# Kernel tuning notes

Measured on AMD Instinct MI355X. Metric: run time of the kernel, lower is better.

The kernel has to match this reference:

```python
import jax, jax.numpy as jnp
import numpy as np

SD = 4            # sqrt of capsule dim (matrix pose)
STRIDE = 2
LN_EPS = 1e-5


def _unfold(x, k, s):
    # x: [B, N, H, W, A] -> patches [B, N, k, k, Ho, Wo, A]  (matches torch unfold+permute)
    B, N, H, W, A = x.shape
    Ho = (H - k) // s + 1
    Wo = (W - k) // s + 1
    ih = np.arange(Ho)[:, None] * s + np.arange(k)   # [Ho, k]
    iw = np.arange(Wo)[:, None] * s + np.arange(k)   # [Wo, k]
    p = x[:, :, ih]               # [B, N, Ho, k, W, A]
    p = p[:, :, :, :, iw]         # [B, N, Ho, k, Wo, k, A]
    return p.transpose(0, 1, 3, 5, 2, 4, 6)


def _layer_norm(v, g, b):
    mu = jnp.mean(v, axis=-1, keepdims=True)
    var = jnp.mean(jnp.square(v - mu), axis=-1, keepdims=True)
    return (v - mu) * jax.lax.rsqrt(var + LN_EPS) * g + b


def setup_inputs() -> dict:
    key = jax.random.key(0)
    k0, k1, k2 = jax.random.split(key, 3)
    B, N, H, W, A = 64, 32, 16, 16, 16     # batch, in caps, spatial, pose dim
    K, M, D = 3, 32, 16                     # kernel, out caps (conv), out pose dim
    Ho = Wo = (H - K) // STRIDE + 1         # 7
    Nfc, Cls = M * Ho * Wo, 10              # 1568 fc input caps, 10 classes
    x = jax.random.normal(k0, (B, N, H, W, A), dtype=jnp.float32)
    c_conv = np.sqrt(M / (SD * N * K * K)).astype(np.float32)
    w_conv = c_conv * jax.random.normal(k1, (K, K, N, SD, SD, M), dtype=jnp.float32)
    c_fc = np.sqrt(Cls / (SD * Nfc)).astype(np.float32)
    w_fc = c_fc * jax.random.normal(k2, (Nfc, SD, SD, Cls), dtype=jnp.float32)
    return {
        "x": x, "w_conv": w_conv, "w_fc": w_fc,
        "ln1_g": jnp.ones((D,), jnp.float32), "ln1_b": jnp.zeros((D,), jnp.float32),
        "ln2_g": jnp.ones((D,), jnp.float32), "ln2_b": jnp.zeros((D,), jnp.float32),
        "num_routing": 3,
    }


def reference(x, w_conv, w_fc, ln1_g, ln1_b, ln2_g, ln2_b, num_routing):
    B = x.shape[0]
    K, _, N, _, _, M = w_conv.shape
    D = SD * SD
    scale = 1.0 / np.sqrt(D)

    # ---------------- CapsuleCONV (matrix pose) ----------------
    patches = _unfold(x, K, STRIDE)                       # [B,N,K,K,Ho,Wo,A]
    Ho, Wo = patches.shape[4], patches.shape[5]
    inp = patches.reshape(B, N, K, K, Ho, Wo, SD, SD)     # bnklhwax

    # pass 0: uniform routing prior (softmax of zeros) == 1/M
    v = jnp.einsum('bnklhwax,klnxdm->bmhwad', inp, w_conv) / M
    v = _layer_norm(v.reshape(B, M, Ho, Wo, D), ln1_g, ln1_b)
    for _ in range(num_routing - 1):
        v4 = v.reshape(B, M, Ho, Wo, SD, SD)
        logits = jnp.einsum('bnklhwax,klnxdm,bmhwad->bnklmhw', inp, w_conv, v4) * scale
        qk = jax.nn.softmax(logits, axis=4)
        qk = qk / (jnp.sum(qk, axis=4, keepdims=True) + 1e-10)
        v = jnp.einsum('bnklmhw,bnklhwax,klnxdm->bmhwad', qk, inp, w_conv)
        v = _layer_norm(v.reshape(B, M, Ho, Wo, D), ln1_g, ln1_b)

    # ---------------- CapsuleFC (matrix pose) ----------------
    # [B,M,Ho,Wo,D] -> permute(0,4,1,2,3) -> flatten -> [B, M*Ho*Wo, D]
    fc_in = v.transpose(0, 4, 1, 2, 3).reshape(B, D, M * Ho * Wo).transpose(0, 2, 1)
    Nfc, Cls = w_fc.shape[0], w_fc.shape[3]
    _in = fc_in.reshape(B, Nfc, SD, SD)                   # bnax

    u = jnp.einsum('bnax,nxdm->bmad', _in, w_fc) / Cls
    u = _layer_norm(u.reshape(B, Cls, D), ln2_g, ln2_b)
    for _ in range(num_routing - 1):
        u4 = u.reshape(B, Cls, SD, SD)
        logits = jnp.einsum('bnax,nxdm,bmad->bnm', _in, w_fc, u4) * scale
        qk = jax.nn.softmax(logits, axis=2)
        qk = qk / (jnp.sum(qk, axis=2, keepdims=True) + 1e-10)
        u = jnp.einsum('bnm,bnax,nxdm->bmad', qk, _in, w_fc)
        u = _layer_norm(u.reshape(B, Cls, D), ln2_g, ln2_b)

    return u  # [B, num_classes, out_d_capsules]
```

## Files before the change

### kernel.cpp

```cpp
#include <hip/hip_runtime.h>
#include <hip/hip_bf16.h>


#define LN_EPS 1e-5f

typedef _Float16 h2 __attribute__((ext_vector_type(2)));

__device__ __forceinline__ unsigned packh2(float a, float b) {
    const unsigned short ua = __builtin_bit_cast(unsigned short, (_Float16)a);
    const unsigned short ub = __builtin_bit_cast(unsigned short, (_Float16)b);
    return (unsigned)ua | ((unsigned)ub << 16);
}

__device__ __forceinline__ float fdot2u(unsigned a, unsigned b, float c) {
#if __has_builtin(__builtin_amdgcn_fdot2)
    return __builtin_amdgcn_fdot2(__builtin_bit_cast(h2, a),
                                  __builtin_bit_cast(h2, b), c, false);
#else
    const h2 ha = __builtin_bit_cast(h2, a), hb = __builtin_bit_cast(h2, b);
    return fmaf((float)ha.x, (float)hb.x, fmaf((float)ha.y, (float)hb.y, c));
#endif
}

__global__ __launch_bounds__(256) void transpose_wconv(
    const float* __restrict__ wconv, unsigned short* __restrict__ wTh)
{
    const int i = blockIdx.x * 256 + threadIdx.x;
    if (i < 147456) {
        const int x = i & 3, d = (i >> 2) & 3, mm = (i >> 4) & 31, r = i >> 9;
        const int n = r / 9, kl = r % 9;
        const float v = wconv[((kl * 32 + n) * 16 + x * 4 + d) * 32 + mm];
        wTh[i] = __builtin_bit_cast(unsigned short, (_Float16)v);
    }
}
__global__ __launch_bounds__(256) void transpose_wfc(
    const float* __restrict__ wfc, float* __restrict__ wT2b)
{
    const int j = blockIdx.x * 256 + threadIdx.x;
    if (j < 401408) {
        const int xd = j & 15, mm = (j >> 4) & 15, n = j >> 8;
        const int x = xd >> 2, dd = xd & 3;
        wT2b[j] = (mm < 10) ? wfc[((n * 4 + x) * 4 + dd) * 10 + mm] : 0.f;
    }
}
__global__ __launch_bounds__(256) void transpose_weights(
    const float* __restrict__ wconv, const float* __restrict__ wfc,
    unsigned short* __restrict__ wTh, float* __restrict__ wT2b)
{
    const int blk = blockIdx.x;
    if (blk < 576) {
        const int i = blk * 256 + threadIdx.x;
        if (i < 147456) {
            const int x = i & 3, d = (i >> 2) & 3, mm = (i >> 4) & 31, r = i >> 9;
            const int n = r / 9, kl = r % 9;
            const float v = wconv[((kl * 32 + n) * 16 + x * 4 + d) * 32 + mm];
            wTh[i] = __builtin_bit_cast(unsigned short, (_Float16)v);
        }
    } else {
        const int j = (blk - 576) * 256 + threadIdx.x;
        if (j < 401408) {
            const int xd = j & 15, mm = (j >> 4) & 15, n = j >> 8;
            const int x = xd >> 2, dd = xd & 3;
            wT2b[j] = (mm < 10) ? wfc[((n * 4 + x) * 4 + dd) * 10 + mm] : 0.f;
        }
    }
}

__global__ __launch_bounds__(256, 4) void conv_routing_kernel(
    const float* __restrict__ x,
    const unsigned short* __restrict__ wTh,
    const float* __restrict__ ln1g,
    const float* __restrict__ ln1b,
    const int*   __restrict__ nroute,
    float* __restrict__ vout)
{
    __shared__ unsigned short s_inp[288][16];
    __shared__ float s_v[32][17];
    __shared__ float s_red[2][32][17];

    const int tid = threadIdx.x;
    const int m   = tid & 31;
    const int g   = (tid >> 5) & 7;
    const int lw  = tid >> 6;
    const int site = blockIdx.x;
    const int b = site / 49, hw = site % 49;
    const int h = hw / 7, w = hw % 7;

    for (int i = tid; i < 1152; i += 256) {
        const int row = i >> 2, q = i & 3;
        const int n = row / 9, kl = row % 9;
        const int k = kl / 3, l = kl % 3;
        const float4 val = *(const float4*)(
            x + ((((b * 32 + n) * 16 + (2 * h + k)) * 16 + (2 * w + l)) * 16 + q * 4));
        uint2 p;
        p.x = packh2(val.x, val.y);
        p.y = packh2(val.z, val.w);
        *(uint2*)(&s_inp[row][q * 4]) = p;
    }
    __syncthreads();

    const int R = *nroute;
    const int nkl0 = g * 36;
    const unsigned short* const wp0 = wTh + (nkl0 * 32 + m) * 16;

    for (int pass = 0; pass < R; ++pass) {
        float vn[16];
#pragma unroll
        for (int i = 0; i < 16; ++i) vn[i] = 0.f;

        if (pass == 0) {
            const unsigned short* wp = wp0;
            for (int t = 0; t < 36; ++t, wp += 512) {
                const uint4 wa = *(const uint4*)(wp);
                const uint4 wb = *(const uint4*)(wp + 8);
                const unsigned wu[8] = { wa.x, wa.y, wa.z, wa.w, wb.x, wb.y, wb.z, wb.w };
                const uint4* rp = (const uint4*)(&s_inp[nkl0 + t][0]);
                const uint4 ua = rp[0], ub = rp[1];
                const unsigned iu[8] = { ua.x, ua.y, ua.z, ua.w, ub.x, ub.y, ub.z, ub.w };
#pragma unroll
                for (int a = 0; a < 4; ++a) {
#pragma unroll
                    for (int d = 0; d < 4; ++d) {
                        vn[a * 4 + d] = fdot2u(iu[a * 2], wu[d * 2],
                            fdot2u(iu[a * 2 + 1], wu[d * 2 + 1], vn[a * 4 + d]));
                    }
                }
            }
        } else {
            const unsigned short* wp = wp0;
            for (int j = 0; j < 18; ++j, wp += 1024) {
                const uint4 wa0 = *(const uint4*)(wp);
                const uint4 wb0 = *(const uint4*)(wp + 8);
                const uint4 wa1 = *(const uint4*)(wp + 512);
                const uint4 wb1 = *(const uint4*)(wp + 520);
                const unsigned wu0[8] = { wa0.x, wa0.y, wa0.z, wa0.w, wb0.x, wb0.y, wb0.z, wb0.w };
                const unsigned wu1[8] = { wa1.x, wa1.y, wa1.z, wa1.w, wb1.x, wb1.y, wb1.z, wb1.w };
                const uint4* rp0 = (const uint4*)(&s_inp[nkl0 + 2 * j][0]);
                const uint4* rp1 = (const uint4*)(&s_inp[nkl0 + 2 * j + 1][0]);
                const uint4 ua0 = rp0[0], ub0 = rp0[1];
                const uint4 ua1 = rp1[0], ub1 = rp1[1];
                const unsigned iu0[8] = { ua0.x, ua0.y, ua0.z, ua0.w, ub0.x, ub0.y, ub0.z, ub0.w };
                const unsigned iu1[8] = { ua1.x, ua1.y, ua1.z, ua1.w, ub1.x, ub1.y, ub1.z, ub1.w };

                float uh0[16], uh1[16];
#pragma unroll
                for (int a = 0; a < 4; ++a) {
#pragma unroll
                    for (int d = 0; d < 4; ++d) {
                        uh0[a * 4 + d] = fdot2u(iu0[a * 2], wu0[d * 2],
                            fdot2u(iu0[a * 2 + 1], wu0[d * 2 + 1], 0.f));
                        uh1[a * 4 + d] = fdot2u(iu1[a * 2], wu1[d * 2],
                            fdot2u(iu1[a * 2 + 1], wu1[d * 2 + 1], 0.f));
                    }
                }

                const float* vcp = &s_v[m][0];
                float p0 = 0.f, p1 = 0.f, q0 = 0.f, q1 = 0.f;
#pragma unroll
                for (int i = 0; i < 16; i += 2) {
                    const float c0 = vcp[i], c1 = vcp[i + 1];
                    p0 = fmaf(uh0[i], c0, p0);
                    q0 = fmaf(uh0[i + 1], c1, q0);
                    p1 = fmaf(uh1[i], c0, p1);
                    q1 = fmaf(uh1[i + 1], c1, q1);
                }
                const float e0 = __expf((p0 + q0) * 0.25f);
                const float e1 = __expf((p1 + q1) * 0.25f);

                float sm0 = e0, sm1 = e1;
#pragma unroll
                for (int off = 16; off >= 1; off >>= 1) {
                    const float r0 = __shfl_xor(sm0, off, 32);
                    const float r1 = __shfl_xor(sm1, off, 32);
                    sm0 += r0;
                    sm1 += r1;
                }
                const float qk0 = e0 * __builtin_amdgcn_rcpf(sm0 * (1.f + 1e-10f));
                const float qk1 = e1 * __builtin_amdgcn_rcpf(sm1 * (1.f + 1e-10f));
#pragma unroll
                for (int i = 0; i < 16; ++i) {
                    vn[i] = fmaf(qk0, uh0[i], vn[i]);
                    vn[i] = fmaf(qk1, uh1[i], vn[i]);
                }
            }
        }

#pragma unroll
        for (int i = 0; i < 16; ++i) vn[i] += __shfl_xor(vn[i], 32, 64);

        if (lw >= 2) {
#pragma unroll
            for (int i = 0; i < 16; ++i) s_red[lw - 2][m][i] = vn[i];
        }
        __syncthreads();
        if (lw < 2) {
#pragma unroll
            for (int i = 0; i < 16; ++i) vn[i] += s_red[lw][m][i];
            if (lw == 1) {
#pragma unroll
                for (int i = 0; i < 16; ++i) s_red[1][m][i] = vn[i];
            }
        }
        __syncthreads();
        if (lw == 0) {
#pragma unroll
            for (int i = 0; i < 16; ++i) vn[i] += s_red[1][m][i];
            const float scale = pass ? 1.f : (1.f / 32.f);
            float mu = 0.f;
#pragma unroll
            for (int i = 0; i < 16; ++i) { vn[i] *= scale; mu += vn[i]; }
            mu *= (1.f / 16.f);
            float var = 0.f;
#pragma unroll
            for (int i = 0; i < 16; ++i) {
                const float d0 = vn[i] - mu;
                var = fmaf(d0, d0, var);
            }
            var *= (1.f / 16.f);
            const float inv = rsqrtf(var + LN_EPS);
#pragma unroll
            for (int i = 0; i < 16; ++i)
                s_v[m][i] = (vn[i] - mu) * inv * ln1g[i] + ln1b[i];
        }
        __syncthreads();
    }

    for (int p = tid; p < 512; p += 256) {
        const int mm = p >> 4, i = p & 15;
        vout[((b * 32 + mm) * 49 + hw) * 16 + i] = s_v[mm][i];
    }
}

__global__ __launch_bounds__(256, 4) void fc_pass(
    const float* __restrict__ fcin,
    const float* __restrict__ wT2b,
    const float* __restrict__ prev,
    const float* __restrict__ ln2g,
    const float* __restrict__ ln2b,
    const int*   __restrict__ nroute,
    const int    pass,
    float* __restrict__ pout)
{
    __shared__ float s_red[4][16][17];
    __shared__ float s_u[16][17];

    const int R = *nroute;
    if (pass >= R) return;
    const int blk = blockIdx.x;
    const int b = blk >> 3, c = blk & 7;
    const int tid = threadIdx.x;
    const int ml = tid & 15, grp = tid >> 4;
    const int wv = tid >> 6;

    float ur[16];
    if (pass) {
        const int mlf = tid >> 4, ii = tid & 15;
        float s = 0.f;
#pragma unroll
        for (int c2 = 0; c2 < 8; ++c2)
            s += prev[((b * 8 + c2) * 16 + mlf) * 16 + ii];
        if (pass == 1) s *= 0.1f;
        float mu = s;
#pragma unroll
        for (int off = 8; off >= 1; off >>= 1) mu += __shfl_xor(mu, off, 16);
        mu *= (1.f / 16.f);
        const float d0 = s - mu;
        float var = d0 * d0;
#pragma unroll
        for (int off = 8; off >= 1; off >>= 1) var += __shfl_xor(var, off, 16);
        var *= (1.f / 16.f);
        s_u[mlf][ii] = (s - mu) * rsqrtf(var + LN_EPS) * ln2g[ii] + ln2b[ii];
        __syncthreads();
#pragma unroll
        for (int i = 0; i < 16; ++i) ur[i] = s_u[ml][i];
    }

    const float* fb = fcin + (b * 1568 + c * 196) * 16;
    const float* wb = wT2b + (c * 196 * 16) * 16;

    float un[16];
#pragma unroll
    for (int i = 0; i < 16; ++i) un[i] = 0.f;

    for (int t = 0; t < 13; ++t) {
        const int off = t * 16 + grp;
        if (off >= 196) break;
        float iv[16], wv_[16];
        const float* ip = fb + off * 16;
        const float* wp = wb + (off * 16 + ml) * 16;
#pragma unroll
        for (int q = 0; q < 4; ++q) {
            *(float4*)(&iv[q * 4]) = *(const float4*)(ip + q * 4);
            *(float4*)(&wv_[q * 4]) = *(const float4*)(wp + q * 4);
        }
        float vote[16];
#pragma unroll
        for (int a = 0; a < 4; ++a) {
#pragma unroll
            for (int d = 0; d < 4; ++d) {
                float acc = iv[a * 4 + 0] * wv_[0 + d];
                acc = fmaf(iv[a * 4 + 1], wv_[4 + d], acc);
                acc = fmaf(iv[a * 4 + 2], wv_[8 + d], acc);
                acc = fmaf(iv[a * 4 + 3], wv_[12 + d], acc);
                vote[a * 4 + d] = acc;
            }
        }
        if (pass == 0) {
#pragma unroll
            for (int i = 0; i < 16; ++i) un[i] += vote[i];
        } else {
            float l0 = vote[0] * ur[0], l1 = vote[1] * ur[1];
            float l2 = vote[2] * ur[2], l3 = vote[3] * ur[3];
#pragma unroll
            for (int i = 4; i < 16; i += 4) {
                l0 = fmaf(vote[i + 0], ur[i + 0], l0);
                l1 = fmaf(vote[i + 1], ur[i + 1], l1);
                l2 = fmaf(vote[i + 2], ur[i + 2], l2);
                l3 = fmaf(vote[i + 3], ur[i + 3], l3);
            }
            const float lg = ((l0 + l1) + (l2 + l3)) * 0.25f;
            float e = __expf(lg);
            if (ml >= 10) e = 0.f;
            float sm = e;
#pragma unroll
            for (int off2 = 8; off2 >= 1; off2 >>= 1)
                sm += __shfl_xor(sm, off2, 16);
            const float qk = e * __builtin_amdgcn_rcpf(sm * (1.f + 1e-10f));
#pragma unroll
            for (int i = 0; i < 16; ++i) un[i] = fmaf(qk, vote[i], un[i]);
        }
    }

#pragma unroll
    for (int i = 0; i < 16; ++i) {
        un[i] += __shfl_xor(un[i], 16, 64);
        un[i] += __shfl_xor(un[i], 32, 64);
    }
    if ((tid & 63) < 16) {
#pragma unroll
        for (int i = 0; i < 16; ++i) s_red[wv][ml][i] = un[i];
    }
    __syncthreads();
    {
        const int mlf = tid >> 4, i = tid & 15;
        const float s = s_red[0][mlf][i] + s_red[1][mlf][i]
                      + s_red[2][mlf][i] + s_red[3][mlf][i];
        pout[(blk * 16 + mlf) * 16 + i] = s;
    }
}

__global__ __launch_bounds__(256) void fc_final(
    const float* __restrict__ pA,
    const float* __restrict__ pB,
    const float* __restrict__ ln2g,
    const float* __restrict__ ln2b,
    const int*   __restrict__ nroute,
    float* __restrict__ out)
{
    const int R = *nroute;
    const float* P = ((R - 1) & 1) ? pB : pA;
    const int b = blockIdx.x;
    const int tid = threadIdx.x;
    const int i = tid & 15, ml = tid >> 4;

    float s = 0.f;
#pragma unroll
    for (int c = 0; c < 8; ++c)
        s += P[((b * 8 + c) * 16 + ml) * 16 + i];
    if (R == 1) s *= 0.1f;

    float mu = s;
#pragma unroll
    for (int off = 8; off >= 1; off >>= 1) mu += __shfl_xor(mu, off, 16);
    mu *= (1.f / 16.f);
    const float d0 = s - mu;
    float var = d0 * d0;
#pragma unroll
    for (int off = 8; off >= 1; off >>= 1) var += __shfl_xor(var, off, 16);
    var *= (1.f / 16.f);
    const float r = (s - mu) * rsqrtf(var + LN_EPS) * ln2g[i] + ln2b[i];

    if (ml < 10) out[(b * 10 + ml) * 16 + i] = r;
}

__global__ __launch_bounds__(256, 4) void fc_partial(
    const float* __restrict__ fcin, const float* __restrict__ wT2b,
    const float* __restrict__ u, const int* __restrict__ nroute,
    const int pass, float* __restrict__ partial)
{
    __shared__ float s_red[4][16][17];
    const int R = *nroute;
    if (pass >= R) return;
    const int blk = blockIdx.x;
    const int b = blk >> 3, c = blk & 7;
    const int tid = threadIdx.x;
    const int ml = tid & 15, grp = tid >> 4;
    const int wv = tid >> 6;
    const float* fb = fcin + (b * 1568 + c * 196) * 16;
    const float* wb = wT2b + (c * 196 * 16) * 16;

    float un[16];
#pragma unroll
    for (int i = 0; i < 16; ++i) un[i] = 0.f;
    float ur[16];
    if (pass) {
#pragma unroll
        for (int q = 0; q < 4; ++q)
            *(float4*)(&ur[q * 4]) = *(const float4*)(u + (b * 16 + ml) * 16 + q * 4);
    }
    for (int t = 0; t < 13; ++t) {
        const int off = t * 16 + grp;
        if (off >= 196) break;
        float iv[16], wv_[16];
        const float* ip = fb + off * 16;
        const float* wp = wb + (off * 16 + ml) * 16;
#pragma unroll
        for (int q = 0; q < 4; ++q) {
            *(float4*)(&iv[q * 4]) = *(const float4*)(ip + q * 4);
            *(float4*)(&wv_[q * 4]) = *(const float4*)(wp + q * 4);
        }
        float vote[16];
#pragma unroll
        for (int a = 0; a < 4; ++a) {
#pragma unroll
            for (int d = 0; d < 4; ++d) {
                float acc = iv[a * 4 + 0] * wv_[0 + d];
                acc = fmaf(iv[a * 4 + 1], wv_[4 + d], acc);
                acc = fmaf(iv[a * 4 + 2], wv_[8 + d], acc);
                acc = fmaf(iv[a * 4 + 3], wv_[12 + d], acc);
                vote[a * 4 + d] = acc;
            }
        }
        if (pass == 0) {
#pragma unroll
            for (int i = 0; i < 16; ++i) un[i] += vote[i];
        } else {
            float l0 = vote[0] * ur[0], l1 = vote[1] * ur[1];
            float l2 = vote[2] * ur[2], l3 = vote[3] * ur[3];
#pragma unroll
            for (int i = 4; i < 16; i += 4) {
                l0 = fmaf(vote[i + 0], ur[i + 0], l0);
                l1 = fmaf(vote[i + 1], ur[i + 1], l1);
                l2 = fmaf(vote[i + 2], ur[i + 2], l2);
                l3 = fmaf(vote[i + 3], ur[i + 3], l3);
            }
            const float lg = ((l0 + l1) + (l2 + l3)) * 0.25f;
            float e = __expf(lg);
            if (ml >= 10) e = 0.f;
            float sm = e;
#pragma unroll
            for (int off2 = 8; off2 >= 1; off2 >>= 1)
                sm += __shfl_xor(sm, off2, 16);
            const float qk = e * __builtin_amdgcn_rcpf(sm * (1.f + 1e-10f));
#pragma unroll
            for (int i = 0; i < 16; ++i) un[i] = fmaf(qk, vote[i], un[i]);
        }
    }
#pragma unroll
    for (int i = 0; i < 16; ++i) {
        un[i] += __shfl_xor(un[i], 16, 64);
        un[i] += __shfl_xor(un[i], 32, 64);
    }
    if ((tid & 63) < 16) {
#pragma unroll
        for (int i = 0; i < 16; ++i) s_red[wv][ml][i] = un[i];
    }
    __syncthreads();
    {
        const int mlf = tid >> 4, i = tid & 15;
        const float s = s_red[0][mlf][i] + s_red[1][mlf][i]
                      + s_red[2][mlf][i] + s_red[3][mlf][i];
        partial[(blk * 16 + mlf) * 16 + i] = s;
    }
}

__global__ __launch_bounds__(256) void fc_combine(
    const float* __restrict__ partial, const float* __restrict__ ln2g,
    const float* __restrict__ ln2b, const int* __restrict__ nroute,
    const int pass, float* __restrict__ u, float* __restrict__ out)
{
    const int R = *nroute;
    if (pass >= R) return;
    const int b = blockIdx.x;
    const int tid = threadIdx.x;
    const int i = tid & 15, ml = tid >> 4;
    float s = 0.f;
#pragma unroll
    for (int c = 0; c < 8; ++c)
        s += partial[((b * 8 + c) * 16 + ml) * 16 + i];
    if (pass == 0) s *= 0.1f;
    float mu = s;
#pragma unroll
    for (int off = 8; off >= 1; off >>= 1) mu += __shfl_xor(mu, off, 16);
    mu *= (1.f / 16.f);
    const float d0 = s - mu;
    float var = d0 * d0;
#pragma unroll
    for (int off = 8; off >= 1; off >>= 1) var += __shfl_xor(var, off, 16);
    var *= (1.f / 16.f);
    const float r = (s - mu) * rsqrtf(var + LN_EPS) * ln2g[i] + ln2b[i];
    u[(b * 16 + ml) * 16 + i] = r;
    if (pass == R - 1 && ml < 10) out[(b * 10 + ml) * 16 + i] = r;
}

extern "C" void kernel_launch(void* const* d_in, const int* in_sizes, int n_in,
                              void* d_out, int out_size, void* d_ws, size_t ws_size,
                              hipStream_t stream) {
    const float* x     = (const float*)d_in[0];
    const float* wconv = (const float*)d_in[1];
    const float* wfc   = (const float*)d_in[2];
    const float* ln1g  = (const float*)d_in[3];
    const float* ln1b  = (const float*)d_in[4];
    const float* ln2g  = (const float*)d_in[5];
    const float* ln2b  = (const float*)d_in[6];
    const int*   nrt   = (const int*)d_in[7];
    float* out = (float*)d_out;

    float* vout = (float*)d_ws;

    if (ws_size >= 9076736) {
        float* wT2b = (float*)((char*)d_ws + 6422528);
        float* pA   = (float*)((char*)d_ws + 8028160);
        float* pB   = (float*)((char*)d_ws + 8552448);
        unsigned short* wTh = (unsigned short*)pA;

        hipLaunchKernelGGL(transpose_weights, dim3(2144), dim3(256), 0, stream,
                           wconv, wfc, wTh, wT2b);
        hipLaunchKernelGGL(conv_routing_kernel, dim3(3136), dim3(256), 0, stream,
                           x, wTh, ln1g, ln1b, nrt, vout);
        hipLaunchKernelGGL(fc_pass, dim3(512), dim3(256), 0, stream,
                           vout, wT2b, (const float*)nullptr, ln2g, ln2b, nrt, 0, pA);
        hipLaunchKernelGGL(fc_pass, dim3(512), dim3(256), 0, stream,
                           vout, wT2b, (const float*)pA, ln2g, ln2b, nrt, 1, pB);
        hipLaunchKernelGGL(fc_pass, dim3(512), dim3(256), 0, stream,
                           vout, wT2b, (const float*)pB, ln2g, ln2b, nrt, 2, pA);
        hipLaunchKernelGGL(fc_final, dim3(64), dim3(256), 0, stream,
                           pA, pB, ln2g, ln2b, nrt, out);
    } else {
        unsigned short* wTh = (unsigned short*)((char*)d_ws + 6422528);
        float* wT2b    = (float*)((char*)d_ws + 6422528);
        float* ubuf    = (float*)((char*)d_ws + 8028160);
        float* partial = (float*)((char*)d_ws + 8093696);

        hipLaunchKernelGGL(transpose_wconv, dim3(576), dim3(256), 0, stream,
                           wconv, wTh);
        hipLaunchKernelGGL(conv_routing_kernel, dim3(3136), dim3(256), 0, stream,
                           x, wTh, ln1g, ln1b, nrt, vout);
        hipLaunchKernelGGL(transpose_wfc, dim3(1568), dim3(256), 0, stream,
                           wfc, wT2b);
        for (int pass = 0; pass < 3; ++pass) {
            hipLaunchKernelGGL(fc_partial, dim3(512), dim3(256), 0, stream,
                               vout, wT2b, ubuf, nrt, pass, partial);
            hipLaunchKernelGGL(fc_combine, dim3(64), dim3(256), 0, stream,
                               partial, ln2g, ln2b, nrt, pass, ubuf, out);
        }
    }
}
```

Measured before the change: 307.1 us.

## Compute capsule conv routing votes with MFMA 16x16x32 f16 instructions

Replaces the per-thread fdot2 vote computation in the conv routing kernel with MFMA 16x16x32 f16 matrix instructions. Each wave takes 72 input rows, and the A operand is zero-padded through a dummy zero row so only the diagonal k-slice holds data. Weight fragments are double-buffered from global memory across iterations. The cross-wave reduction and layer norm are reorganised around the MFMA output layout, and the occupancy hint drops to 2 blocks. The change keeps routing logits and softmax in registers via shuffles, but most of the MFMA K dimension is padding, so much of its throughput is wasted.

```diff
diff --git a/kernel.cpp b/kernel.cpp
--- a/kernel.cpp
+++ b/kernel.cpp
@@ -5,21 +5,13 @@
 #define LN_EPS 1e-5f
 
 typedef _Float16 h2 __attribute__((ext_vector_type(2)));
+typedef _Float16 half8_t __attribute__((ext_vector_type(8)));
+typedef float float4_t __attribute__((ext_vector_type(4)));
 
 __device__ __forceinline__ unsigned packh2(float a, float b) {
     const unsigned short ua = __builtin_bit_cast(unsigned short, (_Float16)a);
     const unsigned short ub = __builtin_bit_cast(unsigned short, (_Float16)b);
     return (unsigned)ua | ((unsigned)ub << 16);
-}
-
-__device__ __forceinline__ float fdot2u(unsigned a, unsigned b, float c) {
-#if __has_builtin(__builtin_amdgcn_fdot2)
-    return __builtin_amdgcn_fdot2(__builtin_bit_cast(h2, a),
-                                  __builtin_bit_cast(h2, b), c, false);
-#else
-    const h2 ha = __builtin_bit_cast(h2, a), hb = __builtin_bit_cast(h2, b);
-    return fmaf((float)ha.x, (float)hb.x, fmaf((float)ha.y, (float)hb.y, c));
-#endif
 }
 
 __global__ __launch_bounds__(256) void transpose_wconv(
@@ -66,7 +58,7 @@
     }
 }
 
-__global__ __launch_bounds__(256, 4) void conv_routing_kernel(
+__global__ __launch_bounds__(256, 2) void conv_routing_kernel(
     const float* __restrict__ x,
     const unsigned short* __restrict__ wTh,
     const float* __restrict__ ln1g,
@@ -74,14 +66,21 @@
     const int*   __restrict__ nroute,
     float* __restrict__ vout)
 {
-    __shared__ unsigned short s_inp[288][16];
-    __shared__ float s_v[32][17];
-    __shared__ float s_red[2][32][17];
+    __shared__ unsigned short s_inp[289][16];
+    __shared__ float s_v2[32][16];
+    __shared__ float s_part[4][16][36];
 
     const int tid = threadIdx.x;
-    const int m   = tid & 31;
-    const int g   = (tid >> 5) & 7;
-    const int lw  = tid >> 6;
+    const int wv  = tid >> 6;
+    const int l   = tid & 63;
+    const int hi  = l >> 4;
+    const int c   = l & 15;
+    const int msub = l & 3;
+    const int dq   = c >> 2;
+    const int aj   = c >> 2;
+    const int aa   = c & 3;
+    const bool partA = (aj == hi);
+
     const int site = blockIdx.x;
     const int b = site / 49, hw = site % 49;
     const int h = hw / 7, w = hw % 7;
@@ -89,145 +88,159 @@
     for (int i = tid; i < 1152; i += 256) {
         const int row = i >> 2, q = i & 3;
         const int n = row / 9, kl = row % 9;
-        const int k = kl / 3, l = kl % 3;
+        const int k = kl / 3, lw2 = kl % 3;
         const float4 val = *(const float4*)(
-            x + ((((b * 32 + n) * 16 + (2 * h + k)) * 16 + (2 * w + l)) * 16 + q * 4));
+            x + ((((b * 32 + n) * 16 + (2 * h + k)) * 16 + (2 * w + lw2)) * 16 + q * 4));
         uint2 p;
         p.x = packh2(val.x, val.y);
         p.y = packh2(val.z, val.w);
         *(uint2*)(&s_inp[row][q * 4]) = p;
     }
+    if (tid < 4) {
+        uint2 z; z.x = 0u; z.y = 0u;
+        *(uint2*)(&s_inp[288][tid * 4]) = z;
+    }
     __syncthreads();
 
     const int R = *nroute;
-    const int nkl0 = g * 36;
-    const unsigned short* const wp0 = wTh + (nkl0 * 32 + m) * 16;
+    const int rowBase = wv * 72;
+
+    const int aOffPart = aj * 32 + aa * 8;
+    const int aOffZero = 288 * 32 + aa * 8;
+    const unsigned short* const bpl =
+        wTh + ((rowBase + hi) * 32 + msub) * 16 + dq * 4;
+
+    const float4_t z4 = {0.f, 0.f, 0.f, 0.f};
 
     for (int pass = 0; pass < R; ++pass) {
-        float vn[16];
-#pragma unroll
-        for (int i = 0; i < 16; ++i) vn[i] = 0.f;
-
-        if (pass == 0) {
-            const unsigned short* wp = wp0;
-            for (int t = 0; t < 36; ++t, wp += 512) {
-                const uint4 wa = *(const uint4*)(wp);
-                const uint4 wb = *(const uint4*)(wp + 8);
-                const unsigned wu[8] = { wa.x, wa.y, wa.z, wa.w, wb.x, wb.y, wb.z, wb.w };
-                const uint4* rp = (const uint4*)(&s_inp[nkl0 + t][0]);
-                const uint4 ua = rp[0], ub = rp[1];
-                const unsigned iu[8] = { ua.x, ua.y, ua.z, ua.w, ub.x, ub.y, ub.z, ub.w };
-#pragma unroll
-                for (int a = 0; a < 4; ++a) {
-#pragma unroll
-                    for (int d = 0; d < 4; ++d) {
-                        vn[a * 4 + d] = fdot2u(iu[a * 2], wu[d * 2],
-                            fdot2u(iu[a * 2 + 1], wu[d * 2 + 1], vn[a * 4 + d]));
-                    }
+        float4_t vr[8];
+        if (pass) {
+#pragma unroll
+            for (int t = 0; t < 8; ++t)
+                vr[t] = *(const float4_t*)(&s_v2[4 * t + msub][dq * 4]);
+        }
+
+        float4_t acc[8];
+#pragma unroll
+        for (int t = 0; t < 8; ++t) acc[t] = z4;
+
+        uint4 Bbuf[2][8];
+#pragma unroll
+        for (int s = 0; s < 2; ++s)
+#pragma unroll
+            for (int t = 0; t < 8; ++t) {
+                Bbuf[s][t].z = 0u; Bbuf[s][t].w = 0u;
+            }
+#pragma unroll
+        for (int t = 0; t < 8; ++t) {
+            const uint2 bv = *(const uint2*)(bpl + t * 64);
+            Bbuf[0][t].x = bv.x; Bbuf[0][t].y = bv.y;
+        }
+
+#pragma unroll 2
+        for (int q = 0; q < 18; ++q) {
+            const int rowq = rowBase + q * 4;
+            const int addrA = partA ? (rowq * 32 + aOffPart) : aOffZero;
+            const uint2 av = *(const uint2*)((const char*)(&s_inp[0][0]) + addrA);
+            uint4 au; au.x = av.x; au.y = av.y; au.z = 0u; au.w = 0u;
+            const half8_t a8 = __builtin_bit_cast(half8_t, au);
+
+            if (q < 17) {
+                const unsigned short* bp2 = bpl + (q + 1) * 2048;
+#pragma unroll
+                for (int t = 0; t < 8; ++t) {
+                    const uint2 bv = *(const uint2*)(bp2 + t * 64);
+                    Bbuf[(q + 1) & 1][t].x = bv.x;
+                    Bbuf[(q + 1) & 1][t].y = bv.y;
                 }
             }
-        } else {
-            const unsigned short* wp = wp0;
-            for (int j = 0; j < 18; ++j, wp += 1024) {
-                const uint4 wa0 = *(const uint4*)(wp);
-                const uint4 wb0 = *(const uint4*)(wp + 8);
-                const uint4 wa1 = *(const uint4*)(wp + 512);
-                const uint4 wb1 = *(const uint4*)(wp + 520);
-                const unsigned wu0[8] = { wa0.x, wa0.y, wa0.z, wa0.w, wb0.x, wb0.y, wb0.z, wb0.w };
-                const unsigned wu1[8] = { wa1.x, wa1.y, wa1.z, wa1.w, wb1.x, wb1.y, wb1.z, wb1.w };
-                const uint4* rp0 = (const uint4*)(&s_inp[nkl0 + 2 * j][0]);
-                const uint4* rp1 = (const uint4*)(&s_inp[nkl0 + 2 * j + 1][0]);
-                const uint4 ua0 = rp0[0], ub0 = rp0[1];
-                const uint4 ua1 = rp1[0], ub1 = rp1[1];
-                const unsigned iu0[8] = { ua0.x, ua0.y, ua0.z, ua0.w, ub0.x, ub0.y, ub0.z, ub0.w };
-                const unsigned iu1[8] = { ua1.x, ua1.y, ua1.z, ua1.w, ub1.x, ub1.y, ub1.z, ub1.w };
-
-                float uh0[16], uh1[16];
-#pragma unroll
-                for (int a = 0; a < 4; ++a) {
-#pragma unroll
-                    for (int d = 0; d < 4; ++d) {
-                        uh0[a * 4 + d] = fdot2u(iu0[a * 2], wu0[d * 2],
-                            fdot2u(iu0[a * 2 + 1], wu0[d * 2 + 1], 0.f));
-                        uh1[a * 4 + d] = fdot2u(iu1[a * 2], wu1[d * 2],
-                            fdot2u(iu1[a * 2 + 1], wu1[d * 2 + 1], 0.f));
-                    }
+
+            if (pass == 0) {
+#pragma unroll
+                for (int t = 0; t < 8; ++t) {
+                    const half8_t b8 = __builtin_bit_cast(half8_t, Bbuf[q & 1][t]);
+                    acc[t] = __builtin_amdgcn_mfma_f32_16x16x32_f16(a8, b8, acc[t], 0, 0, 0);
                 }
-
-                const float* vcp = &s_v[m][0];
-                float p0 = 0.f, p1 = 0.f, q0 = 0.f, q1 = 0.f;
-#pragma unroll
-                for (int i = 0; i < 16; i += 2) {
-                    const float c0 = vcp[i], c1 = vcp[i + 1];
-                    p0 = fmaf(uh0[i], c0, p0);
-                    q0 = fmaf(uh0[i + 1], c1, q0);
-                    p1 = fmaf(uh1[i], c0, p1);
-                    q1 = fmaf(uh1[i + 1], c1, q1);
+            } else {
+                float4_t ct[8];
+#pragma unroll
+                for (int t = 0; t < 8; ++t) {
+                    const half8_t b8 = __builtin_bit_cast(half8_t, Bbuf[q & 1][t]);
+                    ct[t] = __builtin_amdgcn_mfma_f32_16x16x32_f16(a8, b8, z4, 0, 0, 0);
                 }
-                const float e0 = __expf((p0 + q0) * 0.25f);
-                const float e1 = __expf((p1 + q1) * 0.25f);
-
-                float sm0 = e0, sm1 = e1;
-#pragma unroll
-                for (int off = 16; off >= 1; off >>= 1) {
-                    const float r0 = __shfl_xor(sm0, off, 32);
-                    const float r1 = __shfl_xor(sm1, off, 32);
-                    sm0 += r0;
-                    sm1 += r1;
+                float e[8];
+#pragma unroll
+                for (int t = 0; t < 8; ++t) {
+                    float pt = ct[t][0] * vr[t][0];
+                    pt = fmaf(ct[t][1], vr[t][1], pt);
+                    pt = fmaf(ct[t][2], vr[t][2], pt);
+                    pt = fmaf(ct[t][3], vr[t][3], pt);
+                    pt += __shfl_xor(pt, 4, 64);
+                    pt += __shfl_xor(pt, 8, 64);
+                    e[t] = __expf(pt * 0.25f);
                 }
-                const float qk0 = e0 * __builtin_amdgcn_rcpf(sm0 * (1.f + 1e-10f));
-                const float qk1 = e1 * __builtin_amdgcn_rcpf(sm1 * (1.f + 1e-10f));
-#pragma unroll
-                for (int i = 0; i < 16; ++i) {
-                    vn[i] = fmaf(qk0, uh0[i], vn[i]);
-                    vn[i] = fmaf(qk1, uh1[i], vn[i]);
+                float zsum = ((e[0] + e[1]) + (e[2] + e[3]))
+                           + ((e[4] + e[5]) + (e[6] + e[7]));
+                zsum += __shfl_xor(zsum, 1, 64);
+                zsum += __shfl_xor(zsum, 2, 64);
+                const float rq = __builtin_amdgcn_rcpf(zsum * (1.f + 1e-10f));
+#pragma unroll
+                for (int t = 0; t < 8; ++t) {
+                    const float qk = e[t] * rq;
+                    acc[t] = acc[t] + ct[t] * qk;
                 }
             }
         }
 
 #pragma unroll
-        for (int i = 0; i < 16; ++i) vn[i] += __shfl_xor(vn[i], 32, 64);
-
-        if (lw >= 2) {
-#pragma unroll
-            for (int i = 0; i < 16; ++i) s_red[lw - 2][m][i] = vn[i];
+        for (int t = 0; t < 8; ++t) {
+#pragma unroll
+            for (int r = 0; r < 4; ++r) {
+                float v0 = acc[t][r];
+                v0 += __shfl_xor(v0, 16, 64);
+                v0 += __shfl_xor(v0, 32, 64);
+                acc[t][r] = v0;
+            }
+        }
+        if (l < 16) {
+#pragma unroll
+            for (int t = 0; t < 8; ++t)
+                *(float4_t*)(&s_part[wv][l][t * 4]) = acc[t];
         }
         __syncthreads();
-        if (lw < 2) {
-#pragma unroll
-            for (int i = 0; i < 16; ++i) vn[i] += s_red[lw][m][i];
-            if (lw == 1) {
-#pragma unroll
-                for (int i = 0; i < 16; ++i) s_red[1][m][i] = vn[i];
-            }
-        }
-        __syncthreads();
-        if (lw == 0) {
-#pragma unroll
-            for (int i = 0; i < 16; ++i) vn[i] += s_red[1][m][i];
-            const float scale = pass ? 1.f : (1.f / 32.f);
-            float mu = 0.f;
-#pragma unroll
-            for (int i = 0; i < 16; ++i) { vn[i] *= scale; mu += vn[i]; }
-            mu *= (1.f / 16.f);
-            float var = 0.f;
-#pragma unroll
-            for (int i = 0; i < 16; ++i) {
-                const float d0 = vn[i] - mu;
-                var = fmaf(d0, d0, var);
-            }
-            var *= (1.f / 16.f);
-            const float inv = rsqrtf(var + LN_EPS);
-#pragma unroll
-            for (int i = 0; i < 16; ++i)
-                s_v[m][i] = (vn[i] - mu) * inv * ln1g[i] + ln1b[i];
+
+        if (tid < 128) {
+            const int m = tid >> 2, p = tid & 3;
+            const int lo = p * 4 + (m & 3), slot = (m >> 2) * 4;
+            float4_t xs = *(const float4_t*)(&s_part[0][lo][slot]);
+            xs = xs + *(const float4_t*)(&s_part[1][lo][slot]);
+            xs = xs + *(const float4_t*)(&s_part[2][lo][slot]);
+            xs = xs + *(const float4_t*)(&s_part[3][lo][slot]);
+            if (pass == 0) xs = xs * (1.f / 32.f);
+
+            float s0 = (xs[0] + xs[1]) + (xs[2] + xs[3]);
+            s0 += __shfl_xor(s0, 1, 64);
+            s0 += __shfl_xor(s0, 2, 64);
+            const float mu = s0 * (1.f / 16.f);
+            float vvar = 0.f;
+#pragma unroll
+            for (int a = 0; a < 4; ++a) {
+                const float d0 = xs[a] - mu;
+                vvar = fmaf(d0, d0, vvar);
+            }
+            vvar += __shfl_xor(vvar, 1, 64);
+            vvar += __shfl_xor(vvar, 2, 64);
+            const float inv = rsqrtf(vvar * (1.f / 16.f) + LN_EPS);
+#pragma unroll
+            for (int a = 0; a < 4; ++a)
+                s_v2[m][p * 4 + a] = (xs[a] - mu) * inv * ln1g[a * 4 + p] + ln1b[a * 4 + p];
         }
         __syncthreads();
     }
 
     for (int p = tid; p < 512; p += 256) {
         const int mm = p >> 4, i = p & 15;
-        vout[((b * 32 + mm) * 49 + hw) * 16 + i] = s_v[mm][i];
+        vout[((b * 32 + mm) * 49 + hw) * 16 + i] = s_v2[mm][(i & 3) * 4 + (i >> 2)];
     }
 }
 
```

Result: slower. 384.3 us (+25.1%).
